# Kernel tuning notes

Measured on AMD Instinct MI355X. Metric: run time of the kernel, lower is better.

## Reference

```python
import jax, jax.numpy as jnp
import numpy as np
from jax import lax

D = 768
C = 37          # num_classes + 1
PAD_ID = C - 1  # label_init puts '[PAD]' last
B, S = 128, 512


def setup_inputs() -> dict:
    key = jax.random.key(0)
    ks = jax.random.split(key, 8)
    x = jax.random.normal(ks[0], (B, S, D), dtype=jnp.float32)
    W = jax.random.normal(ks[1], (D, C), dtype=jnp.float32) * (1.0 / np.sqrt(D))
    b = jnp.zeros((C,), dtype=jnp.float32)
    start = jax.random.uniform(ks[2], (C,), minval=-0.1, maxval=0.1)
    end = jax.random.uniform(ks[3], (C,), minval=-0.1, maxval=0.1)
    trans = jax.random.uniform(ks[4], (C, C), minval=-0.1, maxval=0.1)
    labels = jax.random.randint(ks[5], (B, S), 0, C)
    lengths = jax.random.randint(ks[6], (B,), 16, S + 1)
    mask = (jnp.arange(S)[None, :] < lengths[:, None])  # first column always True
    return {"x": x, "W": W, "b": b, "start": start, "end": end,
            "trans": trans, "labels": labels, "mask": mask}


def _crf(emissions, labels, mask, start, end, trans):
    # time-major, as in pytorch-crf
    em = jnp.transpose(emissions, (1, 0, 2))      # [S, B, C]
    tg = labels.T                                  # [S, B]
    mkb = mask.T                                   # [S, B] bool
    mkf = mkb.astype(em.dtype)
    bidx = jnp.arange(em.shape[1])

    # ---- gold path score ----
    score0 = start[tg[0]] + em[0, bidx, tg[0]]
    def step_score(carry, inp):
        prev_tag, s = carry
        e_t, t_t, mf, mb = inp
        s = s + (trans[prev_tag, t_t] + e_t[bidx, t_t]) * mf
        prev_tag = jnp.where(mb, t_t, prev_tag)
        return (prev_tag, s), None
    (last_tag, score), _ = lax.scan(step_score, (tg[0], score0),
                                    (em[1:], tg[1:], mkf[1:], mkb[1:]))
    score = score + end[last_tag]

    # ---- log partition (forward algorithm) ----
    alpha0 = start[None, :] + em[0]               # [B, C]
    def step_norm(alpha, inp):
        e_t, mb = inp
        nxt = jax.nn.logsumexp(alpha[:, :, None] + trans[None, :, :], axis=1) + e_t
        return jnp.where(mb[:, None], nxt, alpha), None
    alpha, _ = lax.scan(step_norm, alpha0, (em[1:], mkb[1:]))
    logZ = jax.nn.logsumexp(alpha + end[None, :], axis=1)
    ll = jnp.sum(score - logZ)                    # reduction='sum'

    # ---- Viterbi decode ----
    ident = jnp.arange(C)[None, :]
    v0 = start[None, :] + em[0]
    def step_vit(v, inp):
        e_t, mb = inp
        cand = v[:, :, None] + trans[None, :, :]  # [B, prev, cur]
        bp = jnp.argmax(cand, axis=1)             # [B, C]
        nxt = jnp.max(cand, axis=1) + e_t
        v = jnp.where(mb[:, None], nxt, v)
        bp = jnp.where(mb[:, None], bp, ident)    # identity at padded steps
        return v, bp
    v, bps = lax.scan(step_vit, v0, (em[1:], mkb[1:]))  # bps: [S-1, B, C]
    last = jnp.argmax(v + end[None, :], axis=1)   # [B]
    def back(tag, bp):
        return bp[bidx, tag], tag
    first, rest = lax.scan(back, last, bps, reverse=True)
    tags = jnp.concatenate([first[None, :], rest], axis=0).T  # [B, S]
    tags = jnp.where(mask, tags, PAD_ID)
    return ll, tags


def reference(x, W, b, start, end, trans, labels, mask):
    emissions = jnp.einsum('bsd,dc->bsc', x, W) + b  # linear head
    log_likelihood, tags = _crf(emissions, labels, mask, start, end, trans)
    return log_likelihood, tags
```

## Files before the change

kernel.cpp:

```cpp
#include <hip/hip_runtime.h>

#define Bq 128
#define Sq 512
#define Cq 37
#define Dq 768
#define VST 40

typedef __attribute__((ext_vector_type(2))) float f32x2;
typedef __attribute__((ext_vector_type(4))) float f32x4;
typedef __attribute__((ext_vector_type(8))) short bf16x8;

static __device__ __forceinline__ f32x2 pk_fma(f32x2 a, f32x2 b, f32x2 c) {
  f32x2 d; asm("v_pk_fma_f32 %0, %1, %2, %3" : "=v"(d) : "v"(a), "v"(b), "v"(c));
  return d;
}
static __device__ __forceinline__ f32x2 pk_add(f32x2 a, f32x2 b) {
  f32x2 d; asm("v_pk_add_f32 %0, %1, %2" : "=v"(d) : "v"(a), "v"(b));
  return d;
}
static __device__ __forceinline__ float bcast(float v, int p) {
  return __int_as_float(__builtin_amdgcn_ds_bpermute(p << 2, __float_as_int(v)));
}

#define REP18(X) X(0)X(1)X(2)X(3)X(4)X(5)X(6)X(7)X(8)X(9)X(10)X(11)X(12)X(13) \
  X(14)X(15)X(16)X(17)
#define REP37(X) X(0)X(1)X(2)X(3)X(4)X(5)X(6)X(7)X(8)X(9)X(10)X(11)X(12)X(13) \
  X(14)X(15)X(16)X(17)X(18)X(19)X(20)X(21)X(22)X(23)X(24)X(25)X(26)X(27)X(28) \
  X(29)X(30)X(31)X(32)X(33)X(34)X(35)X(36)

__global__ __launch_bounds__(256) void prep_kernel(
    const float* __restrict__ W, unsigned short* __restrict__ Wbh,
    unsigned short* __restrict__ Wbl)
{
  int i = blockIdx.x * 256 + threadIdx.x;
  if (i >= 24 * 3 * 64 * 8) return;
  int ks = i / 1536, rem = i % 1536;
  int nt = rem / 512, rem2 = rem % 512;
  int lane = rem2 >> 3, j = rem2 & 7;
  int k = ks * 32 + (lane >> 4) * 8 + j;
  int c = nt * 16 + (lane & 15);
  float w = (c < Cq) ? W[(size_t)k * Cq + c] : 0.f;
  unsigned u = __float_as_uint(w);
  unsigned short h = (unsigned short)(u >> 16);
  float hr = __uint_as_float((unsigned)h << 16);
  float r = w - hr;
  Wbh[i] = h;
  Wbl[i] = (unsigned short)(__float_as_uint(r) >> 16);
}

__global__ __launch_bounds__(256) void emis_kernel(
    const float* __restrict__ x, const unsigned short* __restrict__ Wbh,
    const unsigned short* __restrict__ Wbl, const float* __restrict__ bias,
    float* __restrict__ em)
{
  int tid = threadIdx.x, lane = tid & 63;
  int wv = tid >> 6;
  int tokBase = blockIdx.x * 64 + wv * 16;
  int row = lane & 15, kg = lane >> 4;
  const float* xr = x + (size_t)(tokBase + row) * Dq + kg * 8;
  const bf16x8* Bh = (const bf16x8*)Wbh;
  const bf16x8* Bl = (const bf16x8*)Wbl;
  f32x4 acc0 = {0.f, 0.f, 0.f, 0.f};
  f32x4 acc1 = {0.f, 0.f, 0.f, 0.f};
  f32x4 acc2 = {0.f, 0.f, 0.f, 0.f};

  float4 c0 = *(const float4*)(xr);
  float4 c1 = *(const float4*)(xr + 4);
  for (int ks = 0; ks < 24; ++ks) {
    float4 n0, n1;
    if (ks < 23) {
      n0 = *(const float4*)(xr + (ks + 1) * 32);
      n1 = *(const float4*)(xr + (ks + 1) * 32 + 4);
    }
    float fs0 = c0.x, fs1 = c0.y, fs2 = c0.z, fs3 = c0.w;
    float fs4 = c1.x, fs5 = c1.y, fs6 = c1.z, fs7 = c1.w;
    bf16x8 ah, al;
#define SPLIT(J, V) { unsigned u = __float_as_uint(V); \
    unsigned short h = (unsigned short)(u >> 16); \
    float hr = __uint_as_float((unsigned)h << 16); \
    float rr = (V) - hr; \
    ah[J] = (short)h; al[J] = (short)(__float_as_uint(rr) >> 16); }
    SPLIT(0, fs0) SPLIT(1, fs1) SPLIT(2, fs2) SPLIT(3, fs3)
    SPLIT(4, fs4) SPLIT(5, fs5) SPLIT(6, fs6) SPLIT(7, fs7)
#undef SPLIT
    int fi = (ks * 3) * 64 + lane;
    bf16x8 bh0 = Bh[fi], bh1 = Bh[fi + 64], bh2 = Bh[fi + 128];
    bf16x8 bl0 = Bl[fi], bl1 = Bl[fi + 64], bl2 = Bl[fi + 128];
    acc0 = __builtin_amdgcn_mfma_f32_16x16x32_bf16(al, bh0, acc0, 0, 0, 0);
    acc1 = __builtin_amdgcn_mfma_f32_16x16x32_bf16(al, bh1, acc1, 0, 0, 0);
    acc2 = __builtin_amdgcn_mfma_f32_16x16x32_bf16(al, bh2, acc2, 0, 0, 0);
    acc0 = __builtin_amdgcn_mfma_f32_16x16x32_bf16(ah, bl0, acc0, 0, 0, 0);
    acc1 = __builtin_amdgcn_mfma_f32_16x16x32_bf16(ah, bl1, acc1, 0, 0, 0);
    acc2 = __builtin_amdgcn_mfma_f32_16x16x32_bf16(ah, bl2, acc2, 0, 0, 0);
    acc0 = __builtin_amdgcn_mfma_f32_16x16x32_bf16(ah, bh0, acc0, 0, 0, 0);
    acc1 = __builtin_amdgcn_mfma_f32_16x16x32_bf16(ah, bh1, acc1, 0, 0, 0);
    acc2 = __builtin_amdgcn_mfma_f32_16x16x32_bf16(ah, bh2, acc2, 0, 0, 0);
    c0 = n0; c1 = n1;
  }
  int colc = lane & 15;
#pragma unroll
  for (int r = 0; r < 4; ++r) {
    size_t tok = (size_t)tokBase + kg * 4 + r;
    em[tok * Cq + colc]      = acc0[r] + bias[colc];
    em[tok * Cq + 16 + colc] = acc1[r] + bias[16 + colc];
    if (colc < 5)
      em[tok * Cq + 32 + colc] = acc2[r] + bias[32 + colc];
  }
}

__global__ __launch_bounds__(256) void crf_serial_kernel(
    const float* __restrict__ em, const float* __restrict__ startv,
    const float* __restrict__ endv, const float* __restrict__ trans,
    const int* __restrict__ labels, const unsigned char* __restrict__ maskb,
    float* __restrict__ vhist, float* __restrict__ llp,
    int* __restrict__ lenp, int* __restrict__ lastp)
{
  __shared__ float semm[(Sq + 4) * Cq];
  __shared__ float sexch[128];
  __shared__ float s_score, s_logZ;
  int b = blockIdx.x;
  int tid = threadIdx.x, wid = tid >> 6, lane = tid & 63;
  int cl = lane < Cq ? lane : Cq - 1;

  int esz4 = (maskb[1] == 0) ? 1 : 0;
  int len = 0;
#pragma unroll
  for (int k = 0; k < 8; ++k) {
    size_t t = (size_t)lane + (size_t)k * 64;
    unsigned char mb = esz4 ? maskb[((size_t)b * Sq + t) * 4] : maskb[(size_t)b * Sq + t];
    len += (mb != 0);
  }
#pragma unroll
  for (int off = 32; off; off >>= 1) len += __shfl_xor(len, off);

  const float4* src4 = (const float4*)(em + (size_t)b * Sq * Cq);
  float4* dst4 = (float4*)semm;
  for (int i = tid; i < (Sq * Cq) / 4; i += 256) dst4[i] = src4[i];
  if (tid < 4 * Cq) semm[Sq * Cq + tid] = 0.f;
  __syncthreads();

  const float L2E = 1.4426950408889634f, LN2 = 0.6931471805599453f;

  if (wid == 0) {
    f32x2 E2[18];
#pragma unroll
    for (int i = 0; i < 18; ++i) {
      E2[i].x = exp2f(trans[(2 * i) * Cq + cl] * L2E);
      E2[i].y = exp2f(trans[(2 * i + 1) * Cq + cl] * L2E);
    }
    float E36 = exp2f(trans[36 * Cq + cl] * L2E);
    float* sE = sexch;
    const float4* se4 = (const float4*)sE;
    float a0 = (lane < Cq) ? (startv[cl] + semm[cl]) : -3.0e38f;
    float K0 = bcast(a0, 0);
    float ez = (lane < Cq) ? exp2f((a0 - K0) * L2E) : 0.f;
    int eacc = 0;
    float wA = exp2f(semm[1 * Cq + cl] * L2E), wB = exp2f(semm[2 * Cq + cl] * L2E);
    float wC = exp2f(semm[3 * Cq + cl] * L2E), wD = exp2f(semm[4 * Cq + cl] * L2E);
    for (int t = 1; t < len; ++t) {
      sE[lane] = ez;
      float raw = semm[(t + 4) * Cq + cl];
      float4 gv[10];
#pragma unroll
      for (int q = 0; q < 10; ++q) gv[q] = se4[q];
      int e0 = ((__float_as_int(gv[0].x) >> 23) & 255) - 127;
      float scale = __int_as_float((127 - e0) << 23);
      f32x2 sa = {0.f, 0.f}, sb = {0.f, 0.f};
#define FPK(i) { f32x2 g; \
      if ((i) & 1) { g.x = gv[(i) >> 1].z; g.y = gv[(i) >> 1].w; } \
      else         { g.x = gv[(i) >> 1].x; g.y = gv[(i) >> 1].y; } \
      if ((i) & 1) sb = pk_fma(g, E2[i], sb); else sa = pk_fma(g, E2[i], sa); }
      REP18(FPK)
#undef FPK
      float dot = ((sa.x + sb.x) + (sa.y + sb.y)) + gv[9].x * E36;
      float wcur = wA; wA = wB; wB = wC; wC = wD;
      ez = dot * (wcur * scale);
      eacc += e0;
      wD = exp2f(raw * L2E);
    }
    float xv = (lane < Cq) ? LN2 * (log2f(ez) + (float)eacc) + K0 + endv[cl] : -3.0e38f;
    float mm = xv;
#pragma unroll
    for (int off = 32; off; off >>= 1) mm = fmaxf(mm, __shfl_xor(mm, off));
    float es = exp2f((xv - mm) * L2E);
#pragma unroll
    for (int off = 32; off; off >>= 1) es += __shfl_xor(es, off);
    if (lane == 0) s_logZ = mm + log2f(es) * LN2;
  } else if (wid == 1) {
    f32x2 T2[18];
#pragma unroll
    for (int i = 0; i < 18; ++i) {
      T2[i].x = trans[(2 * i) * Cq + cl];
      T2[i].y = trans[(2 * i + 1) * Cq + cl];
    }
    float T36 = trans[36 * Cq + cl];
    float* sV = sexch + 64;
    const float4* sv4 = (const float4*)sV;
    float v = (lane < Cq) ? (startv[cl] + semm[cl]) : -3.0e38f;
    if (lane < Cq) vhist[((size_t)b * Sq) * VST + cl] = v;
    float emA = semm[1 * Cq + cl], emB = semm[2 * Cq + cl];
    float emC = semm[3 * Cq + cl], emD = semm[4 * Cq + cl];
    for (int t = 1; t < len; ++t) {
      sV[lane] = v;
      float raw = semm[(t + 4) * Cq + cl];
      float4 gv[10];
#pragma unroll
      for (int q = 0; q < 10; ++q) gv[q] = sv4[q];
      float m0 = -3.0e38f, m1 = -3.0e38f, m2 = -3.0e38f, m3 = -3.0e38f;
#define VPK(i) { f32x2 g; \
      if ((i) & 1) { g.x = gv[(i) >> 1].z; g.y = gv[(i) >> 1].w; } \
      else         { g.x = gv[(i) >> 1].x; g.y = gv[(i) >> 1].y; } \
      f32x2 c = pk_add(g, T2[i]); \
      if (((i) & 3) == 0) m0 = fmaxf(fmaxf(m0, c.x), c.y); \
      else if (((i) & 3) == 1) m1 = fmaxf(fmaxf(m1, c.x), c.y); \
      else if (((i) & 3) == 2) m2 = fmaxf(fmaxf(m2, c.x), c.y); \
      else m3 = fmaxf(fmaxf(m3, c.x), c.y); }
      REP18(VPK)
#undef VPK
      float c36 = gv[9].x + T36;
      float best = fmaxf(fmaxf(fmaxf(m0, m1), fmaxf(m2, m3)), c36);
      float emc = emA; emA = emB; emB = emC; emC = emD;
      v = (lane < Cq) ? best + emc : -3.0e38f;
      if (lane < Cq) vhist[((size_t)b * Sq + t) * VST + cl] = v;
      emD = raw;
    }
    float xv = (lane < Cq) ? v + endv[cl] : -3.0e38f;
    int idx = (lane < Cq) ? lane : 1000;
#pragma unroll
    for (int off = 32; off; off >>= 1) {
      float xo = __shfl_xor(xv, off); int io = __shfl_xor(idx, off);
      if (xo > xv || (xo == xv && io < idx)) { xv = xo; idx = io; }
    }
    if (lane == 0) { lastp[b] = idx; lenp[b] = len; }
  } else if (wid == 2) {
    const int* lab = labels + (size_t)b * Sq;
    float sc = 0.f;
#pragma unroll
    for (int k = 0; k < 8; ++k) {
      int t = 1 + lane + k * 64;
      if (t < len) {
        int lp = lab[t - 1], lt = lab[t];
        sc += trans[lp * Cq + lt] + semm[t * Cq + lt];
      }
    }
#pragma unroll
    for (int off = 32; off; off >>= 1) sc += __shfl_xor(sc, off);
    if (lane == 0) {
      int l0 = lab[0], lf = lab[len - 1];
      s_score = sc + startv[l0] + semm[l0] + endv[lf];
    }
  }
  __syncthreads();
  if (tid == 0) llp[b] = s_score - s_logZ;
}

__global__ __launch_bounds__(256) void crf_bp_kernel(
    const float* __restrict__ vhist, const float* __restrict__ trans,
    const int* __restrict__ lenp, unsigned char* __restrict__ bp)
{
  int b = blockIdx.x >> 2, chunk = blockIdx.x & 3;
  int wid = threadIdx.x >> 6, lane = threadIdx.x & 63;
  int cl = lane < Cq ? lane : Cq - 1;
  int len = lenp[b];
#define DECLT(i) float T##i = trans[(i) * Cq + cl];
  REP37(DECLT)
  int tend = 1 + (chunk + 1) * 128; if (tend > len) tend = len;
  int rl9 = lane < VST ? lane : VST - 1;
  for (int t = 1 + chunk * 128 + wid; t < tend; t += 4) {
    float vr = vhist[((size_t)b * Sq + (t - 1)) * VST + rl9];
#define BCASTB(i) float br##i = bcast(vr, (i));
    REP37(BCASTB)
    float best = -3.0e38f; int bi = 0;
#define BARG(i) { float cnd = br##i + T##i; if (cnd > best) { best = cnd; bi = (i); } }
    REP37(BARG)
    if (lane < Cq) bp[((size_t)b * VST + cl) * Sq + t] = (unsigned char)bi;
  }
}

__global__ __launch_bounds__(64) void crf_back_kernel(
    const unsigned char* __restrict__ bp, const int* __restrict__ lenp,
    const int* __restrict__ lastp, float* __restrict__ outp)
{
  int b = blockIdx.x, lane = threadIdx.x;
  int len = __builtin_amdgcn_readfirstlane(lenp[b]);
  int tag = __builtin_amdgcn_readfirstlane(lastp[b]);
  int row = lane < VST ? lane : VST - 1;
  const uint4* src = (const uint4*)(bp + ((size_t)b * VST + row) * Sq);
  unsigned r[128];
#pragma unroll
  for (int k = 0; k < 32; ++k) {
    uint4 q = src[k];
    r[4 * k] = q.x; r[4 * k + 1] = q.y; r[4 * k + 2] = q.z; r[4 * k + 3] = q.w;
  }
  unsigned vt[8];
#pragma unroll
  for (int j = 0; j < 8; ++j) vt[j] = 0u;
  vt[7] = (lane == 63) ? (unsigned)tag : vt[7];
#pragma unroll
  for (int t = 510; t >= 0; --t) {
    int word = __builtin_amdgcn_readlane((int)r[(t + 1) >> 2], tag);
    int nt = (word >> (((t + 1) & 3) * 8)) & 0xff;
    tag = (t + 1 < len) ? nt : tag;
    vt[t >> 6] = (lane == (t & 63)) ? (unsigned)tag : vt[t >> 6];
  }
#pragma unroll
  for (int j = 0; j < 8; ++j) {
    int t = j * 64 + lane;
    float o = (t < len) ? (float)(int)vt[j] : 36.0f;
    outp[(size_t)b * Sq + t] = o;
  }
}

__global__ __launch_bounds__(64) void ll_reduce_kernel(
    const float* __restrict__ llp, float* __restrict__ outp)
{
  int lane = threadIdx.x;
  float s = llp[lane] + llp[lane + 64];
#pragma unroll
  for (int off = 32; off; off >>= 1) s += __shfl_xor(s, off);
  if (lane == 0) outp[0] = s;
}

extern "C" void kernel_launch(void* const* d_in, const int* in_sizes, int n_in,
                              void* d_out, int out_size, void* d_ws, size_t ws_size,
                              hipStream_t stream)
{
  const float* x      = (const float*)d_in[0];
  const float* W      = (const float*)d_in[1];
  const float* bias   = (const float*)d_in[2];
  const float* startv = (const float*)d_in[3];
  const float* endv   = (const float*)d_in[4];
  const float* trans  = (const float*)d_in[5];
  const int*   labels = (const int*)d_in[6];
  const unsigned char* maskb = (const unsigned char*)d_in[7];
  float* out = (float*)d_out;

  char* ws = (char*)d_ws;
  float* em            = (float*)(ws);
  float* vhist         = (float*)(ws + 9699328);
  unsigned char* bpbuf = (unsigned char*)(ws + 20185088);
  float* llp           = (float*)(ws + 22806528);
  int*   lenp          = (int*)(ws + 22807552);
  int*   lastp         = (int*)(ws + 22808064);
  unsigned short* Wbh  = (unsigned short*)(ws + 22808576);
  unsigned short* Wbl  = (unsigned short*)(ws + 22882304);

  prep_kernel<<<144, 256, 0, stream>>>(W, Wbh, Wbl);
  emis_kernel<<<1024, 256, 0, stream>>>(x, Wbh, Wbl, bias, em);
  crf_serial_kernel<<<128, 256, 0, stream>>>(em, startv, endv, trans, labels, maskb,
                                             vhist, llp, lenp, lastp);
  crf_bp_kernel<<<512, 256, 0, stream>>>(vhist, trans, lenp, bpbuf);
  crf_back_kernel<<<128, 64, 0, stream>>>(bpbuf, lenp, lastp, out + 1);
  ll_reduce_kernel<<<1, 64, 0, stream>>>(llp, out);
}
```

Measured before the change: 211.0 us.

## Interleave forward and Viterbi recurrences in one wave with software-pipelined LDS

Merges the forward-algorithm and Viterbi serial recurrences, which previously ran on two separate waves, into a single wave. The wave alternates between the two chains, issuing the LDS exchange write and reads for one chain through inline asm while it computes the other, with explicit lgkmcnt waits. The aim is to hide the LDS round-trip latency of each serial step behind the other chain's arithmetic. In exchange one wave now does twice the ALU work per step and carries more registers, and correctness depends on the hand-written waitcnt accounting.

```diff
diff --git a/kernel.cpp b/kernel.cpp
--- a/kernel.cpp
+++ b/kernel.cpp
@@ -27,6 +27,25 @@
 #define REP37(X) X(0)X(1)X(2)X(3)X(4)X(5)X(6)X(7)X(8)X(9)X(10)X(11)X(12)X(13) \
   X(14)X(15)X(16)X(17)X(18)X(19)X(20)X(21)X(22)X(23)X(24)X(25)X(26)X(27)X(28) \
   X(29)X(30)X(31)X(32)X(33)X(34)X(35)X(36)
+
+#define ISSUE(AW, VAL, BASE, GV, RAW, RADDR)                                   \
+  asm volatile("ds_write_b32 %0, %1" :: "v"(AW), "v"(VAL));                    \
+  asm volatile("ds_read_b128 %0, %1 offset:0"   : "=v"(GV[0]) : "v"(BASE));    \
+  asm volatile("ds_read_b128 %0, %1 offset:16"  : "=v"(GV[1]) : "v"(BASE));    \
+  asm volatile("ds_read_b128 %0, %1 offset:32"  : "=v"(GV[2]) : "v"(BASE));    \
+  asm volatile("ds_read_b128 %0, %1 offset:48"  : "=v"(GV[3]) : "v"(BASE));    \
+  asm volatile("ds_read_b128 %0, %1 offset:64"  : "=v"(GV[4]) : "v"(BASE));    \
+  asm volatile("ds_read_b128 %0, %1 offset:80"  : "=v"(GV[5]) : "v"(BASE));    \
+  asm volatile("ds_read_b128 %0, %1 offset:96"  : "=v"(GV[6]) : "v"(BASE));    \
+  asm volatile("ds_read_b128 %0, %1 offset:112" : "=v"(GV[7]) : "v"(BASE));    \
+  asm volatile("ds_read_b128 %0, %1 offset:128" : "=v"(GV[8]) : "v"(BASE));    \
+  asm volatile("ds_read_b128 %0, %1 offset:144" : "=v"(GV[9]) : "v"(BASE));    \
+  asm volatile("ds_read_b32 %0, %1" : "=v"(RAW) : "v"(RADDR));
+
+#define WAIT12                                                                 \
+  __builtin_amdgcn_sched_barrier(0);                                           \
+  asm volatile("s_waitcnt lgkmcnt(12)");                                       \
+  __builtin_amdgcn_sched_barrier(0);
 
 __global__ __launch_bounds__(256) void prep_kernel(
     const float* __restrict__ W, unsigned short* __restrict__ Wbh,
@@ -72,16 +91,14 @@
       n0 = *(const float4*)(xr + (ks + 1) * 32);
       n1 = *(const float4*)(xr + (ks + 1) * 32 + 4);
     }
-    float fs0 = c0.x, fs1 = c0.y, fs2 = c0.z, fs3 = c0.w;
-    float fs4 = c1.x, fs5 = c1.y, fs6 = c1.z, fs7 = c1.w;
     bf16x8 ah, al;
 #define SPLIT(J, V) { unsigned u = __float_as_uint(V); \
     unsigned short h = (unsigned short)(u >> 16); \
     float hr = __uint_as_float((unsigned)h << 16); \
     float rr = (V) - hr; \
     ah[J] = (short)h; al[J] = (short)(__float_as_uint(rr) >> 16); }
-    SPLIT(0, fs0) SPLIT(1, fs1) SPLIT(2, fs2) SPLIT(3, fs3)
-    SPLIT(4, fs4) SPLIT(5, fs5) SPLIT(6, fs6) SPLIT(7, fs7)
+    SPLIT(0, c0.x) SPLIT(1, c0.y) SPLIT(2, c0.z) SPLIT(3, c0.w)
+    SPLIT(4, c1.x) SPLIT(5, c1.y) SPLIT(6, c1.z) SPLIT(7, c1.w)
 #undef SPLIT
     int fi = (ks * 3) * 64 + lane;
     bf16x8 bh0 = Bh[fi], bh1 = Bh[fi + 64], bh2 = Bh[fi + 128];
@@ -116,7 +133,8 @@
     int* __restrict__ lenp, int* __restrict__ lastp)
 {
   __shared__ float semm[(Sq + 4) * Cq];
-  __shared__ float sexch[128];
+  __shared__ __align__(16) float sexchA[64];
+  __shared__ __align__(16) float sexchB[64];
   __shared__ float s_score, s_logZ;
   int b = blockIdx.x;
   int tid = threadIdx.x, wid = tid >> 6, lane = tid & 63;
@@ -142,97 +160,109 @@
   const float L2E = 1.4426950408889634f, LN2 = 0.6931471805599453f;
 
   if (wid == 0) {
-    f32x2 E2[18];
+    f32x2 E2[18], T2[18];
 #pragma unroll
     for (int i = 0; i < 18; ++i) {
-      E2[i].x = exp2f(trans[(2 * i) * Cq + cl] * L2E);
-      E2[i].y = exp2f(trans[(2 * i + 1) * Cq + cl] * L2E);
+      E2[i][0] = exp2f(trans[(2 * i) * Cq + cl] * L2E);
+      E2[i][1] = exp2f(trans[(2 * i + 1) * Cq + cl] * L2E);
+      T2[i][0] = trans[(2 * i) * Cq + cl];
+      T2[i][1] = trans[(2 * i + 1) * Cq + cl];
     }
     float E36 = exp2f(trans[36 * Cq + cl] * L2E);
-    float* sE = sexch;
-    const float4* se4 = (const float4*)sE;
+    float T36 = trans[36 * Cq + cl];
     float a0 = (lane < Cq) ? (startv[cl] + semm[cl]) : -3.0e38f;
     float K0 = bcast(a0, 0);
     float ez = (lane < Cq) ? exp2f((a0 - K0) * L2E) : 0.f;
     int eacc = 0;
+    float v = a0;
+    if (lane < Cq) vhist[((size_t)b * Sq) * VST + cl] = v;
     float wA = exp2f(semm[1 * Cq + cl] * L2E), wB = exp2f(semm[2 * Cq + cl] * L2E);
     float wC = exp2f(semm[3 * Cq + cl] * L2E), wD = exp2f(semm[4 * Cq + cl] * L2E);
-    for (int t = 1; t < len; ++t) {
-      sE[lane] = ez;
-      float raw = semm[(t + 4) * Cq + cl];
-      float4 gv[10];
-#pragma unroll
-      for (int q = 0; q < 10; ++q) gv[q] = se4[q];
-      int e0 = ((__float_as_int(gv[0].x) >> 23) & 255) - 127;
-      float scale = __int_as_float((127 - e0) << 23);
-      f32x2 sa = {0.f, 0.f}, sb = {0.f, 0.f};
-#define FPK(i) { f32x2 g; \
-      if ((i) & 1) { g.x = gv[(i) >> 1].z; g.y = gv[(i) >> 1].w; } \
-      else         { g.x = gv[(i) >> 1].x; g.y = gv[(i) >> 1].y; } \
-      if ((i) & 1) sb = pk_fma(g, E2[i], sb); else sa = pk_fma(g, E2[i], sa); }
-      REP18(FPK)
-#undef FPK
-      float dot = ((sa.x + sb.x) + (sa.y + sb.y)) + gv[9].x * E36;
-      float wcur = wA; wA = wB; wB = wC; wC = wD;
-      ez = dot * (wcur * scale);
-      eacc += e0;
-      wD = exp2f(raw * L2E);
-    }
-    float xv = (lane < Cq) ? LN2 * (log2f(ez) + (float)eacc) + K0 + endv[cl] : -3.0e38f;
-    float mm = xv;
-#pragma unroll
-    for (int off = 32; off; off >>= 1) mm = fmaxf(mm, __shfl_xor(mm, off));
-    float es = exp2f((xv - mm) * L2E);
-#pragma unroll
-    for (int off = 32; off; off >>= 1) es += __shfl_xor(es, off);
-    if (lane == 0) s_logZ = mm + log2f(es) * LN2;
-  } else if (wid == 1) {
-    f32x2 T2[18];
-#pragma unroll
-    for (int i = 0; i < 18; ++i) {
-      T2[i].x = trans[(2 * i) * Cq + cl];
-      T2[i].y = trans[(2 * i + 1) * Cq + cl];
-    }
-    float T36 = trans[36 * Cq + cl];
-    float* sV = sexch + 64;
-    const float4* sv4 = (const float4*)sV;
-    float v = (lane < Cq) ? (startv[cl] + semm[cl]) : -3.0e38f;
-    if (lane < Cq) vhist[((size_t)b * Sq) * VST + cl] = v;
     float emA = semm[1 * Cq + cl], emB = semm[2 * Cq + cl];
     float emC = semm[3 * Cq + cl], emD = semm[4 * Cq + cl];
+
+    unsigned baseA = (unsigned)(unsigned long long)(&sexchA[0]);
+    unsigned baseB = (unsigned)(unsigned long long)(&sexchB[0]);
+    unsigned aWA = baseA + (unsigned)lane * 4u;
+    unsigned aWB = baseB + (unsigned)lane * 4u;
+    unsigned sBse = (unsigned)(unsigned long long)(&semm[0]);
+    f32x4 gvA[10], gvB[10];
+    float rawA, rawB;
+
+    {
+      unsigned rAddr = sBse + (unsigned)(5 * Cq + cl) * 4u;
+      ISSUE(aWA, ez, baseA, gvA, rawA, rAddr)
+    }
     for (int t = 1; t < len; ++t) {
-      sV[lane] = v;
-      float raw = semm[(t + 4) * Cq + cl];
-      float4 gv[10];
-#pragma unroll
-      for (int q = 0; q < 10; ++q) gv[q] = sv4[q];
-      float m0 = -3.0e38f, m1 = -3.0e38f, m2 = -3.0e38f, m3 = -3.0e38f;
+      {
+        int rb = (t + 4 < len) ? t + 4 : len - 1;
+        unsigned rAddr = sBse + (unsigned)(rb * Cq + cl) * 4u;
+        ISSUE(aWB, v, baseB, gvB, rawB, rAddr)
+      }
+      WAIT12
+      {
+        int e0 = ((__float_as_int(gvA[0][0]) >> 23) & 255) - 127;
+        float scale = __int_as_float((127 - e0) << 23);
+        f32x2 sa = {0.f, 0.f}, sb2 = {0.f, 0.f};
+#define FPK(i) { f32x2 g; \
+        g[0] = gvA[(i) >> 1][((i) & 1) * 2]; \
+        g[1] = gvA[(i) >> 1][((i) & 1) * 2 + 1]; \
+        if ((i) & 1) sb2 = pk_fma(g, E2[i], sb2); else sa = pk_fma(g, E2[i], sa); }
+        REP18(FPK)
+#undef FPK
+        float dot = ((sa[0] + sb2[0]) + (sa[1] + sb2[1])) + gvA[9][0] * E36;
+        float wcur = wA; wA = wB; wB = wC; wC = wD;
+        ez = dot * (wcur * scale);
+        eacc += e0;
+        wD = exp2f(rawA * L2E);
+      }
+      {
+        int ra = (t + 5 < len) ? t + 5 : len - 1;
+        unsigned rAddr = sBse + (unsigned)(ra * Cq + cl) * 4u;
+        ISSUE(aWA, ez, baseA, gvA, rawA, rAddr)
+      }
+      WAIT12
+      {
+        float m0 = -3.0e38f, m1 = -3.0e38f, m2 = -3.0e38f, m3 = -3.0e38f;
 #define VPK(i) { f32x2 g; \
-      if ((i) & 1) { g.x = gv[(i) >> 1].z; g.y = gv[(i) >> 1].w; } \
-      else         { g.x = gv[(i) >> 1].x; g.y = gv[(i) >> 1].y; } \
-      f32x2 c = pk_add(g, T2[i]); \
-      if (((i) & 3) == 0) m0 = fmaxf(fmaxf(m0, c.x), c.y); \
-      else if (((i) & 3) == 1) m1 = fmaxf(fmaxf(m1, c.x), c.y); \
-      else if (((i) & 3) == 2) m2 = fmaxf(fmaxf(m2, c.x), c.y); \
-      else m3 = fmaxf(fmaxf(m3, c.x), c.y); }
-      REP18(VPK)
+        g[0] = gvB[(i) >> 1][((i) & 1) * 2]; \
+        g[1] = gvB[(i) >> 1][((i) & 1) * 2 + 1]; \
+        f32x2 c = pk_add(g, T2[i]); \
+        if (((i) & 3) == 0) m0 = fmaxf(fmaxf(m0, c[0]), c[1]); \
+        else if (((i) & 3) == 1) m1 = fmaxf(fmaxf(m1, c[0]), c[1]); \
+        else if (((i) & 3) == 2) m2 = fmaxf(fmaxf(m2, c[0]), c[1]); \
+        else m3 = fmaxf(fmaxf(m3, c[0]), c[1]); }
+        REP18(VPK)
 #undef VPK
-      float c36 = gv[9].x + T36;
-      float best = fmaxf(fmaxf(fmaxf(m0, m1), fmaxf(m2, m3)), c36);
-      float emc = emA; emA = emB; emB = emC; emC = emD;
-      v = (lane < Cq) ? best + emc : -3.0e38f;
-      if (lane < Cq) vhist[((size_t)b * Sq + t) * VST + cl] = v;
-      emD = raw;
-    }
-    float xv = (lane < Cq) ? v + endv[cl] : -3.0e38f;
-    int idx = (lane < Cq) ? lane : 1000;
-#pragma unroll
-    for (int off = 32; off; off >>= 1) {
-      float xo = __shfl_xor(xv, off); int io = __shfl_xor(idx, off);
-      if (xo > xv || (xo == xv && io < idx)) { xv = xo; idx = io; }
-    }
-    if (lane == 0) { lastp[b] = idx; lenp[b] = len; }
-  } else if (wid == 2) {
+        float c36 = gvB[9][0] + T36;
+        float best = fmaxf(fmaxf(fmaxf(m0, m1), fmaxf(m2, m3)), c36);
+        float emc = emA; emA = emB; emB = emC; emC = emD;
+        v = (lane < Cq) ? best + emc : -3.0e38f;
+        if (lane < Cq) vhist[((size_t)b * Sq + t) * VST + cl] = v;
+        emD = rawB;
+      }
+    }
+    {
+      float xv = (lane < Cq) ? LN2 * (log2f(ez) + (float)eacc) + K0 + endv[cl] : -3.0e38f;
+      float mm = xv;
+#pragma unroll
+      for (int off = 32; off; off >>= 1) mm = fmaxf(mm, __shfl_xor(mm, off));
+      float es = exp2f((xv - mm) * L2E);
+#pragma unroll
+      for (int off = 32; off; off >>= 1) es += __shfl_xor(es, off);
+      if (lane == 0) s_logZ = mm + log2f(es) * LN2;
+    }
+    {
+      float xv = (lane < Cq) ? v + endv[cl] : -3.0e38f;
+      int idx = (lane < Cq) ? lane : 1000;
+#pragma unroll
+      for (int off = 32; off; off >>= 1) {
+        float xo = __shfl_xor(xv, off); int io = __shfl_xor(idx, off);
+        if (xo > xv || (xo == xv && io < idx)) { xv = xo; idx = io; }
+      }
+      if (lane == 0) { lastp[b] = idx; lenp[b] = len; }
+    }
+  } else if (wid == 1) {
     const int* lab = labels + (size_t)b * Sq;
     float sc = 0.f;
 #pragma unroll
```

New measurement: 261.7 us. +24.0%, slower.

## Split CRF forward and Viterbi recursions into bidirectional halves meeting at midpoint

Applied to the files above, without the earlier changes.

The serial CRF recursion is split so that forward-alpha and Viterbi run from the start to the midpoint, while new backward-beta and backward-Viterbi waves run from the end to the midpoint. The two halves are merged at m to form logZ and the best midpoint tag. The backpointer kernel gets a second role that computes forward-pointing backpointers for the second half, and the backtrace walks outward from the midpoint in both directions. This roughly halves the serial dependency chain that dominates latency, at the cost of an extra wave per block, more blocks in the bp kernel, and a longer two-pass backtrace.

```diff
diff --git a/kernel.cpp b/kernel.cpp
--- a/kernel.cpp
+++ b/kernel.cpp
@@ -72,16 +72,14 @@
       n0 = *(const float4*)(xr + (ks + 1) * 32);
       n1 = *(const float4*)(xr + (ks + 1) * 32 + 4);
     }
-    float fs0 = c0.x, fs1 = c0.y, fs2 = c0.z, fs3 = c0.w;
-    float fs4 = c1.x, fs5 = c1.y, fs6 = c1.z, fs7 = c1.w;
     bf16x8 ah, al;
 #define SPLIT(J, V) { unsigned u = __float_as_uint(V); \
     unsigned short h = (unsigned short)(u >> 16); \
     float hr = __uint_as_float((unsigned)h << 16); \
     float rr = (V) - hr; \
     ah[J] = (short)h; al[J] = (short)(__float_as_uint(rr) >> 16); }
-    SPLIT(0, fs0) SPLIT(1, fs1) SPLIT(2, fs2) SPLIT(3, fs3)
-    SPLIT(4, fs4) SPLIT(5, fs5) SPLIT(6, fs6) SPLIT(7, fs7)
+    SPLIT(0, c0.x) SPLIT(1, c0.y) SPLIT(2, c0.z) SPLIT(3, c0.w)
+    SPLIT(4, c1.x) SPLIT(5, c1.y) SPLIT(6, c1.z) SPLIT(7, c1.w)
 #undef SPLIT
     int fi = (ks * 3) * 64 + lane;
     bf16x8 bh0 = Bh[fi], bh1 = Bh[fi + 64], bh2 = Bh[fi + 128];
@@ -108,16 +106,20 @@
   }
 }
 
-__global__ __launch_bounds__(256) void crf_serial_kernel(
+__global__ __launch_bounds__(320) void crf_serial_kernel(
     const float* __restrict__ em, const float* __restrict__ startv,
     const float* __restrict__ endv, const float* __restrict__ trans,
     const int* __restrict__ labels, const unsigned char* __restrict__ maskb,
     float* __restrict__ vhist, float* __restrict__ llp,
-    int* __restrict__ lenp, int* __restrict__ lastp)
+    int* __restrict__ lenp, int* __restrict__ lastp, int* __restrict__ midp)
 {
   __shared__ float semm[(Sq + 4) * Cq];
-  __shared__ float sexch[128];
-  __shared__ float s_score, s_logZ;
+  __shared__ __align__(16) float sxA[64];
+  __shared__ __align__(16) float sxB[64];
+  __shared__ __align__(16) float sxC[64];
+  __shared__ __align__(16) float sxD[64];
+  __shared__ float mrgA[64], mrgB[64], mrgV[64], mrgU[64];
+  __shared__ float s_score;
   int b = blockIdx.x;
   int tid = threadIdx.x, wid = tid >> 6, lane = tid & 63;
   int cl = lane < Cq ? lane : Cq - 1;
@@ -132,10 +134,11 @@
   }
 #pragma unroll
   for (int off = 32; off; off >>= 1) len += __shfl_xor(len, off);
+  int m = len >> 1;
 
   const float4* src4 = (const float4*)(em + (size_t)b * Sq * Cq);
   float4* dst4 = (float4*)semm;
-  for (int i = tid; i < (Sq * Cq) / 4; i += 256) dst4[i] = src4[i];
+  for (int i = tid; i < (Sq * Cq) / 4; i += 320) dst4[i] = src4[i];
   if (tid < 4 * Cq) semm[Sq * Cq + tid] = 0.f;
   __syncthreads();
 
@@ -145,76 +148,110 @@
     f32x2 E2[18];
 #pragma unroll
     for (int i = 0; i < 18; ++i) {
-      E2[i].x = exp2f(trans[(2 * i) * Cq + cl] * L2E);
-      E2[i].y = exp2f(trans[(2 * i + 1) * Cq + cl] * L2E);
+      E2[i][0] = exp2f(trans[(2 * i) * Cq + cl] * L2E);
+      E2[i][1] = exp2f(trans[(2 * i + 1) * Cq + cl] * L2E);
     }
     float E36 = exp2f(trans[36 * Cq + cl] * L2E);
-    float* sE = sexch;
-    const float4* se4 = (const float4*)sE;
+    const float4* se4 = (const float4*)sxA;
     float a0 = (lane < Cq) ? (startv[cl] + semm[cl]) : -3.0e38f;
     float K0 = bcast(a0, 0);
     float ez = (lane < Cq) ? exp2f((a0 - K0) * L2E) : 0.f;
     int eacc = 0;
     float wA = exp2f(semm[1 * Cq + cl] * L2E), wB = exp2f(semm[2 * Cq + cl] * L2E);
     float wC = exp2f(semm[3 * Cq + cl] * L2E), wD = exp2f(semm[4 * Cq + cl] * L2E);
-    for (int t = 1; t < len; ++t) {
-      sE[lane] = ez;
-      float raw = semm[(t + 4) * Cq + cl];
+    for (int t = 1; t <= m; ++t) {
+      sxA[lane] = ez;
+      int tn = (t + 4 <= m) ? t + 4 : m;
+      float raw = semm[tn * Cq + cl];
       float4 gv[10];
 #pragma unroll
       for (int q = 0; q < 10; ++q) gv[q] = se4[q];
       int e0 = ((__float_as_int(gv[0].x) >> 23) & 255) - 127;
       float scale = __int_as_float((127 - e0) << 23);
-      f32x2 sa = {0.f, 0.f}, sb = {0.f, 0.f};
+      f32x2 sa = {0.f, 0.f}, sb2 = {0.f, 0.f};
 #define FPK(i) { f32x2 g; \
-      if ((i) & 1) { g.x = gv[(i) >> 1].z; g.y = gv[(i) >> 1].w; } \
-      else         { g.x = gv[(i) >> 1].x; g.y = gv[(i) >> 1].y; } \
-      if ((i) & 1) sb = pk_fma(g, E2[i], sb); else sa = pk_fma(g, E2[i], sa); }
+      g[0] = ((i) & 1) ? gv[(i) >> 1].z : gv[(i) >> 1].x; \
+      g[1] = ((i) & 1) ? gv[(i) >> 1].w : gv[(i) >> 1].y; \
+      if ((i) & 1) sb2 = pk_fma(g, E2[i], sb2); else sa = pk_fma(g, E2[i], sa); }
       REP18(FPK)
 #undef FPK
-      float dot = ((sa.x + sb.x) + (sa.y + sb.y)) + gv[9].x * E36;
+      float dot = ((sa[0] + sb2[0]) + (sa[1] + sb2[1])) + gv[9].x * E36;
       float wcur = wA; wA = wB; wB = wC; wC = wD;
       ez = dot * (wcur * scale);
       eacc += e0;
       wD = exp2f(raw * L2E);
     }
-    float xv = (lane < Cq) ? LN2 * (log2f(ez) + (float)eacc) + K0 + endv[cl] : -3.0e38f;
-    float mm = xv;
-#pragma unroll
-    for (int off = 32; off; off >>= 1) mm = fmaxf(mm, __shfl_xor(mm, off));
-    float es = exp2f((xv - mm) * L2E);
-#pragma unroll
-    for (int off = 32; off; off >>= 1) es += __shfl_xor(es, off);
-    if (lane == 0) s_logZ = mm + log2f(es) * LN2;
+    mrgA[lane] = (lane < Cq) ? LN2 * (log2f(ez) + (float)eacc) + K0 : -3.0e38f;
   } else if (wid == 1) {
+    f32x2 E2[18];
+#pragma unroll
+    for (int i = 0; i < 18; ++i) {
+      E2[i][0] = exp2f(trans[cl * Cq + 2 * i] * L2E);
+      E2[i][1] = exp2f(trans[cl * Cq + 2 * i + 1] * L2E);
+    }
+    float E36 = exp2f(trans[cl * Cq + 36] * L2E);
+    const float4* se4 = (const float4*)sxB;
+    float b0v = (lane < Cq) ? endv[cl] : -3.0e38f;
+    float KB = bcast(b0v, 0);
+    float bz = (lane < Cq) ? exp2f((b0v - KB) * L2E) : 0.f;
+    int eacc = 0;
+    float wA = exp2f(semm[(len - 1) * Cq + cl] * L2E);
+    float wB = exp2f(semm[(len - 2) * Cq + cl] * L2E);
+    float wC = exp2f(semm[(len - 3) * Cq + cl] * L2E);
+    float wD = exp2f(semm[(len - 4) * Cq + cl] * L2E);
+    for (int t = len - 2; t >= m; --t) {
+      float wcur = wA; wA = wB; wB = wC; wC = wD;
+      float s = bz * wcur;
+      sxB[lane] = s;
+      int tn = (t - 3 > 0) ? t - 3 : 0;
+      float raw = semm[tn * Cq + cl];
+      float4 gv[10];
+#pragma unroll
+      for (int q = 0; q < 10; ++q) gv[q] = se4[q];
+      int e0 = ((__float_as_int(gv[0].x) >> 23) & 255) - 127;
+      float scale = __int_as_float((127 - e0) << 23);
+      f32x2 sa = {0.f, 0.f}, sb2 = {0.f, 0.f};
+#define FPK(i) { f32x2 g; \
+      g[0] = ((i) & 1) ? gv[(i) >> 1].z : gv[(i) >> 1].x; \
+      g[1] = ((i) & 1) ? gv[(i) >> 1].w : gv[(i) >> 1].y; \
+      if ((i) & 1) sb2 = pk_fma(g, E2[i], sb2); else sa = pk_fma(g, E2[i], sa); }
+      REP18(FPK)
+#undef FPK
+      float dot = ((sa[0] + sb2[0]) + (sa[1] + sb2[1])) + gv[9].x * E36;
+      bz = dot * scale;
+      eacc += e0;
+      wD = exp2f(raw * L2E);
+    }
+    mrgB[lane] = (lane < Cq) ? LN2 * (log2f(bz) + (float)eacc) + KB : -3.0e38f;
+  } else if (wid == 2) {
     f32x2 T2[18];
 #pragma unroll
     for (int i = 0; i < 18; ++i) {
-      T2[i].x = trans[(2 * i) * Cq + cl];
-      T2[i].y = trans[(2 * i + 1) * Cq + cl];
+      T2[i][0] = trans[(2 * i) * Cq + cl];
+      T2[i][1] = trans[(2 * i + 1) * Cq + cl];
     }
     float T36 = trans[36 * Cq + cl];
-    float* sV = sexch + 64;
-    const float4* sv4 = (const float4*)sV;
+    const float4* sv4 = (const float4*)sxC;
     float v = (lane < Cq) ? (startv[cl] + semm[cl]) : -3.0e38f;
     if (lane < Cq) vhist[((size_t)b * Sq) * VST + cl] = v;
     float emA = semm[1 * Cq + cl], emB = semm[2 * Cq + cl];
     float emC = semm[3 * Cq + cl], emD = semm[4 * Cq + cl];
-    for (int t = 1; t < len; ++t) {
-      sV[lane] = v;
-      float raw = semm[(t + 4) * Cq + cl];
+    for (int t = 1; t <= m; ++t) {
+      sxC[lane] = v;
+      int tn = (t + 4 <= m) ? t + 4 : m;
+      float raw = semm[tn * Cq + cl];
       float4 gv[10];
 #pragma unroll
       for (int q = 0; q < 10; ++q) gv[q] = sv4[q];
       float m0 = -3.0e38f, m1 = -3.0e38f, m2 = -3.0e38f, m3 = -3.0e38f;
 #define VPK(i) { f32x2 g; \
-      if ((i) & 1) { g.x = gv[(i) >> 1].z; g.y = gv[(i) >> 1].w; } \
-      else         { g.x = gv[(i) >> 1].x; g.y = gv[(i) >> 1].y; } \
+      g[0] = ((i) & 1) ? gv[(i) >> 1].z : gv[(i) >> 1].x; \
+      g[1] = ((i) & 1) ? gv[(i) >> 1].w : gv[(i) >> 1].y; \
       f32x2 c = pk_add(g, T2[i]); \
-      if (((i) & 3) == 0) m0 = fmaxf(fmaxf(m0, c.x), c.y); \
-      else if (((i) & 3) == 1) m1 = fmaxf(fmaxf(m1, c.x), c.y); \
-      else if (((i) & 3) == 2) m2 = fmaxf(fmaxf(m2, c.x), c.y); \
-      else m3 = fmaxf(fmaxf(m3, c.x), c.y); }
+      if (((i) & 3) == 0) m0 = fmaxf(fmaxf(m0, c[0]), c[1]); \
+      else if (((i) & 3) == 1) m1 = fmaxf(fmaxf(m1, c[0]), c[1]); \
+      else if (((i) & 3) == 2) m2 = fmaxf(fmaxf(m2, c[0]), c[1]); \
+      else m3 = fmaxf(fmaxf(m3, c[0]), c[1]); }
       REP18(VPK)
 #undef VPK
       float c36 = gv[9].x + T36;
@@ -224,15 +261,48 @@
       if (lane < Cq) vhist[((size_t)b * Sq + t) * VST + cl] = v;
       emD = raw;
     }
-    float xv = (lane < Cq) ? v + endv[cl] : -3.0e38f;
-    int idx = (lane < Cq) ? lane : 1000;
-#pragma unroll
-    for (int off = 32; off; off >>= 1) {
-      float xo = __shfl_xor(xv, off); int io = __shfl_xor(idx, off);
-      if (xo > xv || (xo == xv && io < idx)) { xv = xo; idx = io; }
-    }
-    if (lane == 0) { lastp[b] = idx; lenp[b] = len; }
-  } else if (wid == 2) {
+    mrgV[lane] = v;
+  } else if (wid == 3) {
+    f32x2 T2[18];
+#pragma unroll
+    for (int i = 0; i < 18; ++i) {
+      T2[i][0] = trans[cl * Cq + 2 * i];
+      T2[i][1] = trans[cl * Cq + 2 * i + 1];
+    }
+    float T36 = trans[cl * Cq + 36];
+    const float4* sv4 = (const float4*)sxD;
+    float u = (lane < Cq) ? endv[cl] : -3.0e38f;
+    if (lane < Cq) vhist[((size_t)b * Sq + (len - 1)) * VST + cl] = u;
+    float emA = semm[(len - 1) * Cq + cl], emB = semm[(len - 2) * Cq + cl];
+    float emC = semm[(len - 3) * Cq + cl], emD = semm[(len - 4) * Cq + cl];
+    for (int t = len - 2; t >= m; --t) {
+      float emc = emA; emA = emB; emB = emC; emC = emD;
+      float s = u + emc;
+      sxD[lane] = s;
+      int tn = (t - 3 > 0) ? t - 3 : 0;
+      float raw = semm[tn * Cq + cl];
+      float4 gv[10];
+#pragma unroll
+      for (int q = 0; q < 10; ++q) gv[q] = sv4[q];
+      float m0 = -3.0e38f, m1 = -3.0e38f, m2 = -3.0e38f, m3 = -3.0e38f;
+#define VPK(i) { f32x2 g; \
+      g[0] = ((i) & 1) ? gv[(i) >> 1].z : gv[(i) >> 1].x; \
+      g[1] = ((i) & 1) ? gv[(i) >> 1].w : gv[(i) >> 1].y; \
+      f32x2 c = pk_add(g, T2[i]); \
+      if (((i) & 3) == 0) m0 = fmaxf(fmaxf(m0, c[0]), c[1]); \
+      else if (((i) & 3) == 1) m1 = fmaxf(fmaxf(m1, c[0]), c[1]); \
+      else if (((i) & 3) == 2) m2 = fmaxf(fmaxf(m2, c[0]), c[1]); \
+      else m3 = fmaxf(fmaxf(m3, c[0]), c[1]); }
+      REP18(VPK)
+#undef VPK
+      float c36 = gv[9].x + T36;
+      float best = fmaxf(fmaxf(fmaxf(m0, m1), fmaxf(m2, m3)), c36);
+      u = (lane < Cq) ? best : -3.0e38f;
+      if (lane < Cq && t > m) vhist[((size_t)b * Sq + t) * VST + cl] = u;
+      emD = raw;
+    }
+    mrgU[lane] = u;
+  } else {
     const int* lab = labels + (size_t)b * Sq;
     float sc = 0.f;
 #pragma unroll
@@ -251,39 +321,89 @@
     }
   }
   __syncthreads();
-  if (tid == 0) llp[b] = s_score - s_logZ;
+  if (wid == 0) {
+    float xv = (lane < Cq) ? mrgA[lane] + mrgB[lane] : -3.0e38f;
+    float mm = xv;
+#pragma unroll
+    for (int off = 32; off; off >>= 1) mm = fmaxf(mm, __shfl_xor(mm, off));
+    float es = exp2f((xv - mm) * L2E);
+#pragma unroll
+    for (int off = 32; off; off >>= 1) es += __shfl_xor(es, off);
+    float logZ = mm + log2f(es) * LN2;
+    float pv = (lane < Cq) ? mrgV[lane] + mrgU[lane] : -3.0e38f;
+    int idx = (lane < Cq) ? lane : 1000;
+#pragma unroll
+    for (int off = 32; off; off >>= 1) {
+      float po = __shfl_xor(pv, off); int io = __shfl_xor(idx, off);
+      if (po > pv || (po == pv && io < idx)) { pv = po; idx = io; }
+    }
+    if (lane == 0) {
+      llp[b] = s_score - logZ;
+      lastp[b] = idx; lenp[b] = len; midp[b] = m;
+    }
+  }
 }
 
 __global__ __launch_bounds__(256) void crf_bp_kernel(
-    const float* __restrict__ vhist, const float* __restrict__ trans,
-    const int* __restrict__ lenp, unsigned char* __restrict__ bp)
-{
-  int b = blockIdx.x >> 2, chunk = blockIdx.x & 3;
+    const float* __restrict__ vhist, const float* __restrict__ em,
+    const float* __restrict__ trans, const int* __restrict__ lenp,
+    const int* __restrict__ midp, unsigned char* __restrict__ bp)
+{
+  int role = blockIdx.x >> 9;
+  int bid = blockIdx.x & 511;
+  int b = bid >> 2, chunk = bid & 3;
   int wid = threadIdx.x >> 6, lane = threadIdx.x & 63;
   int cl = lane < Cq ? lane : Cq - 1;
-  int len = lenp[b];
+  int len = lenp[b], m = midp[b];
+  int rl9 = lane < VST ? lane : VST - 1;
+  if (role == 0) {
 #define DECLT(i) float T##i = trans[(i) * Cq + cl];
-  REP37(DECLT)
-  int tend = 1 + (chunk + 1) * 128; if (tend > len) tend = len;
-  int rl9 = lane < VST ? lane : VST - 1;
-  for (int t = 1 + chunk * 128 + wid; t < tend; t += 4) {
-    float vr = vhist[((size_t)b * Sq + (t - 1)) * VST + rl9];
+    REP37(DECLT)
+#undef DECLT
+    int tend = 1 + (chunk + 1) * 128; if (tend > m + 1) tend = m + 1;
+    for (int t = 1 + chunk * 128 + wid; t < tend; t += 4) {
+      float vr = vhist[((size_t)b * Sq + (t - 1)) * VST + rl9];
 #define BCASTB(i) float br##i = bcast(vr, (i));
-    REP37(BCASTB)
-    float best = -3.0e38f; int bi = 0;
+      REP37(BCASTB)
+#undef BCASTB
+      float best = -3.0e38f; int bi = 0;
 #define BARG(i) { float cnd = br##i + T##i; if (cnd > best) { best = cnd; bi = (i); } }
-    REP37(BARG)
-    if (lane < Cq) bp[((size_t)b * VST + cl) * Sq + t] = (unsigned char)bi;
+      REP37(BARG)
+#undef BARG
+      if (lane < Cq) bp[((size_t)b * VST + cl) * Sq + t] = (unsigned char)bi;
+    }
+  } else {
+#define DECLR(i) float R##i = trans[cl * Cq + (i)];
+    REP37(DECLR)
+#undef DECLR
+    int er = lane < Cq ? lane : 0;
+    int s0 = m + 1 + chunk * 128 + wid;
+    int send = m + 1 + (chunk + 1) * 128; if (send > len) send = len;
+    for (int s = s0; s < send; s += 4) {
+      float uv = vhist[((size_t)b * Sq + s) * VST + rl9];
+      float ev = em[((size_t)b * Sq + s) * Cq + er];
+      float sv = uv + ev;
+#define BCASTB(i) float br##i = bcast(sv, (i));
+      REP37(BCASTB)
+#undef BCASTB
+      float best = -3.0e38f; int bi = 0;
+#define BARG(i) { float cnd = br##i + R##i; if (cnd > best) { best = cnd; bi = (i); } }
+      REP37(BARG)
+#undef BARG
+      if (lane < Cq) bp[((size_t)b * VST + cl) * Sq + s] = (unsigned char)bi;
+    }
   }
 }
 
 __global__ __launch_bounds__(64) void crf_back_kernel(
     const unsigned char* __restrict__ bp, const int* __restrict__ lenp,
-    const int* __restrict__ lastp, float* __restrict__ outp)
+    const int* __restrict__ lastp, const int* __restrict__ midp,
+    float* __restrict__ outp)
 {
   int b = blockIdx.x, lane = threadIdx.x;
   int len = __builtin_amdgcn_readfirstlane(lenp[b]);
-  int tag = __builtin_amdgcn_readfirstlane(lastp[b]);
+  int m = __builtin_amdgcn_readfirstlane(midp[b]);
+  int cstar = __builtin_amdgcn_readfirstlane(lastp[b]);
   int row = lane < VST ? lane : VST - 1;
   const uint4* src = (const uint4*)(bp + ((size_t)b * VST + row) * Sq);
   unsigned r[128];
@@ -295,13 +415,30 @@
   unsigned vt[8];
 #pragma unroll
   for (int j = 0; j < 8; ++j) vt[j] = 0u;
-  vt[7] = (lane == 63) ? (unsigned)tag : vt[7];
-#pragma unroll
-  for (int t = 510; t >= 0; --t) {
-    int word = __builtin_amdgcn_readlane((int)r[(t + 1) >> 2], tag);
-    int nt = (word >> (((t + 1) & 3) * 8)) & 0xff;
-    tag = (t + 1 < len) ? nt : tag;
-    vt[t >> 6] = (lane == (t & 63)) ? (unsigned)tag : vt[t >> 6];
+#pragma unroll
+  for (int j = 0; j < 8; ++j)
+    vt[j] = (lane == (m & 63) && (m >> 6) == j) ? (unsigned)cstar : vt[j];
+  {
+    int tag = cstar;
+#pragma unroll
+    for (int t = 1; t <= 510; ++t) {
+      int word = __builtin_amdgcn_readlane((int)r[t >> 2], tag);
+      int nt = (word >> ((t & 3) * 8)) & 0xff;
+      bool live = (t > m) && (t < len);
+      tag = live ? nt : tag;
+      vt[t >> 6] = (lane == (t & 63) && live) ? (unsigned)tag : vt[t >> 6];
+    }
+  }
+  {
+    int tag = cstar;
+#pragma unroll
+    for (int t = 510; t >= 0; --t) {
+      int word = __builtin_amdgcn_readlane((int)r[(t + 1) >> 2], tag);
+      int nt = (word >> (((t + 1) & 3) * 8)) & 0xff;
+      bool live = (t + 1 <= m);
+      tag = live ? nt : tag;
+      vt[t >> 6] = (lane == (t & 63) && live) ? (unsigned)tag : vt[t >> 6];
+    }
   }
 #pragma unroll
   for (int j = 0; j < 8; ++j) {
@@ -342,14 +479,15 @@
   float* llp           = (float*)(ws + 22806528);
   int*   lenp          = (int*)(ws + 22807552);
   int*   lastp         = (int*)(ws + 22808064);
-  unsigned short* Wbh  = (unsigned short*)(ws + 22808576);
-  unsigned short* Wbl  = (unsigned short*)(ws + 22882304);
+  int*   midp          = (int*)(ws + 22809088);
+  unsigned short* Wbh  = (unsigned short*)(ws + 22809600);
+  unsigned short* Wbl  = (unsigned short*)(ws + 22883328);
 
   prep_kernel<<<144, 256, 0, stream>>>(W, Wbh, Wbl);
   emis_kernel<<<1024, 256, 0, stream>>>(x, Wbh, Wbl, bias, em);
-  crf_serial_kernel<<<128, 256, 0, stream>>>(em, startv, endv, trans, labels, maskb,
-                                             vhist, llp, lenp, lastp);
-  crf_bp_kernel<<<512, 256, 0, stream>>>(vhist, trans, lenp, bpbuf);
-  crf_back_kernel<<<128, 64, 0, stream>>>(bpbuf, lenp, lastp, out + 1);
+  crf_serial_kernel<<<128, 320, 0, stream>>>(em, startv, endv, trans, labels, maskb,
+                                             vhist, llp, lenp, lastp, midp);
+  crf_bp_kernel<<<1024, 256, 0, stream>>>(vhist, em, trans, lenp, midp, bpbuf);
+  crf_back_kernel<<<128, 64, 0, stream>>>(bpbuf, lenp, lastp, midp, out + 1);
   ll_reduce_kernel<<<1, 64, 0, stream>>>(llp, out);
 }
```

Measured after the change: 203.6 us. -3.5%, faster.
